# Optimization experiments

Measured on AMD Instinct MI355X. Metric: run time of the kernel, lower is better.

## Reference

```python
import jax, jax.numpy as jnp
import numpy as np

B, T, I, H, O = 1024, 512, 4, 128, 4


def setup_inputs() -> dict:
    key = jax.random.key(0)
    ks = jax.random.split(key, 7)
    s_ih = 1.0 / np.sqrt(H)
    return {
        "x": jax.random.normal(ks[0], (B, T, I), dtype=jnp.float32),
        "W_ih": jax.random.uniform(ks[1], (4 * H, I), jnp.float32, -s_ih, s_ih),
        "W_hh": jax.random.uniform(ks[2], (4 * H, H), jnp.float32, -s_ih, s_ih),
        "b_ih": jax.random.uniform(ks[3], (4 * H,), jnp.float32, -s_ih, s_ih),
        "b_hh": jax.random.uniform(ks[4], (4 * H,), jnp.float32, -s_ih, s_ih),
        "W_fc": jax.random.uniform(ks[5], (O, H), jnp.float32, -s_ih, s_ih),
        "b_fc": jax.random.uniform(ks[6], (O,), jnp.float32, -s_ih, s_ih),
    }


def _lstm_last_hidden(x, W_ih, W_hh, b_ih, b_hh):
    """Single-layer LSTM (PyTorch gate order i,f,g,o); returns h_T of shape (B,H)."""
    Bn = x.shape[0]
    Hn = W_hh.shape[1]
    # Precompute input contributions for all timesteps: (T, B, 4H)
    x_proj = jnp.einsum('bti,gi->tbg', x, W_ih) + (b_ih + b_hh)

    def step(carry, xp_t):
        h, c = carry
        gates = xp_t + h @ W_hh.T  # (B, 4H)
        i_g, f_g, g_g, o_g = jnp.split(gates, 4, axis=-1)
        i_g = jax.nn.sigmoid(i_g)
        f_g = jax.nn.sigmoid(f_g)
        g_g = jnp.tanh(g_g)
        o_g = jax.nn.sigmoid(o_g)
        c = f_g * c + i_g * g_g
        h = o_g * jnp.tanh(c)
        return (h, c), None

    h0 = jnp.zeros((Bn, Hn), x.dtype)
    c0 = jnp.zeros((Bn, Hn), x.dtype)
    (h_T, _), _ = jax.lax.scan(step, (h0, c0), x_proj)
    return h_T


def reference(x, W_ih, W_hh, b_ih, b_hh, W_fc, b_fc):
    # out, _ = lstm(x); last = out[:, -1]; dropout (eval/identity); fc(last)
    last = _lstm_last_hidden(x, W_ih, W_hh, b_ih, b_hh)
    return last @ W_fc.T + b_fc
```

## Files before the change

### kernel.cpp

```cpp
#include <hip/hip_runtime.h>
#include <hip/hip_bf16.h>


#define Tlen 512
#define Iin  4
#define Hdim 128
#define Odim 4

typedef __attribute__((ext_vector_type(8))) short bf16x8;
typedef __attribute__((ext_vector_type(4))) float f32x4;
typedef __attribute__((ext_vector_type(2))) unsigned uint2v;

__device__ __forceinline__ short f2bf(float f) {
  union { float f; unsigned u; } v; v.f = f;
  unsigned u = v.u;
  return (short)((u + 0x7FFFu + ((u >> 16) & 1u)) >> 16);
}
__device__ __forceinline__ unsigned cvt_pk_bf16(float lo, float hi) {
  unsigned r;
  asm("v_cvt_pk_bf16_f32 %0, %1, %2" : "=v"(r) : "v"(lo), "v"(hi));
  return r;
}
__device__ __forceinline__ float ex2(float x) { return __builtin_amdgcn_exp2f(x); }
__device__ __forceinline__ float rcp_(float x) { return __builtin_amdgcn_rcpf(x); }

__global__ __launch_bounds__(512, 2) void lstm_kernel(
    const float* __restrict__ x, const float* __restrict__ W_ih,
    const float* __restrict__ W_hh, const float* __restrict__ b_ih,
    const float* __restrict__ b_hh, const float* __restrict__ W_fc,
    const float* __restrict__ b_fc, float* __restrict__ out) {
  __shared__ alignas(16) short Albuf[2][16][168];
  __shared__ float hfin[16][Hdim];

  const int tid  = threadIdx.x;
  const int wid  = tid >> 6;
  const int lane = tid & 63;
  const int m16  = lane & 15;
  const int grp  = lane >> 4;
  const int bbase = blockIdx.x * 16;
  const float L2E = 1.4426950408889634f;

  bf16x8 Wf[4][5];
  f32x4  c0[4];
#pragma unroll
  for (int q = 0; q < 4; ++q) {
    const float sc = (q == 2) ? 2.0f * L2E : L2E;
    const int gm = q * 128 + wid * 16 + m16;
#pragma unroll
    for (int kc = 0; kc < 4; ++kc) {
      const float* src = W_hh + (size_t)gm * Hdim + kc * 32 + grp * 8;
      bf16x8 w;
#pragma unroll
      for (int e = 0; e < 8; ++e) w[e] = f2bf(src[e] * sc);
      Wf[q][kc] = w;
    }
    bf16x8 w4 = {0, 0, 0, 0, 0, 0, 0, 0};
    if (grp == 0) {
#pragma unroll
      for (int e = 0; e < 4; ++e) w4[e] = f2bf(W_ih[gm * Iin + e] * sc);
    }
    Wf[q][4] = w4;
#pragma unroll
    for (int r = 0; r < 4; ++r) {
      const int gr = q * 128 + wid * 16 + grp * 4 + r;
      c0[q][r] = (b_ih[gr] + b_hh[gr]) * sc;
    }
  }

  for (int i = tid; i < 2 * 16 * 168; i += 512) ((short*)Albuf)[i] = 0;
  __syncthreads();
  if (wid == 0 && lane < 16) {
    const float* xs = x + (size_t)(bbase + m16) * (Tlen * Iin);
    uint2v p;
    p[0] = cvt_pk_bf16(xs[0], xs[1]);
    p[1] = cvt_pk_bf16(xs[2], xs[3]);
    *(uint2v*)&Albuf[0][m16][128] = p;
  }
  __syncthreads();

  float c4[4] = {0.f, 0.f, 0.f, 0.f};
  float hl[4] = {0.f, 0.f, 0.f, 0.f};

  for (int t = 0; t < Tlen; ++t) {
    const int cur = t & 1, nxt = cur ^ 1;

    f32x4 xv = {0.f, 0.f, 0.f, 0.f};
    const bool doX = (wid == 0) && (lane < 16) && (t + 1 < Tlen);
    if (doX)
      xv = *(const f32x4*)(x + (size_t)(bbase + m16) * (Tlen * Iin) + (t + 1) * Iin);

    bf16x8 b[5];
#pragma unroll
    for (int kc = 0; kc < 5; ++kc)
      b[kc] = *(const bf16x8*)&Albuf[cur][m16][kc * 32 + grp * 8];

    f32x4 acc[4];
#pragma unroll
    for (int q = 0; q < 4; ++q)
      acc[q] = __builtin_amdgcn_mfma_f32_16x16x32_bf16(Wf[q][0], b[0], c0[q], 0, 0, 0);
#pragma unroll
    for (int kc = 1; kc < 5; ++kc)
#pragma unroll
      for (int q = 0; q < 4; ++q)
        acc[q] = __builtin_amdgcn_mfma_f32_16x16x32_bf16(Wf[q][kc], b[kc], acc[q], 0, 0, 0);

#pragma unroll
    for (int r = 0; r < 4; ++r) {
      float ig = rcp_(1.0f + ex2(-acc[0][r]));
      float fg = rcp_(1.0f + ex2(-acc[1][r]));
      float gt = __builtin_fmaf(2.0f, rcp_(1.0f + ex2(-acc[2][r])), -1.0f);
      float og = rcp_(1.0f + ex2(-acc[3][r]));
      float c  = __builtin_fmaf(fg, c4[r], ig * gt);
      c4[r] = c;
      float tc = __builtin_fmaf(2.0f, rcp_(1.0f + ex2(-2.8853900817779268f * c)), -1.0f);
      hl[r] = og * tc;
    }
    {
      uint2v p;
      p[0] = cvt_pk_bf16(hl[0], hl[1]);
      p[1] = cvt_pk_bf16(hl[2], hl[3]);
      *(uint2v*)&Albuf[nxt][m16][wid * 16 + grp * 4] = p;
    }
    if (doX) {
      uint2v p;
      p[0] = cvt_pk_bf16(xv[0], xv[1]);
      p[1] = cvt_pk_bf16(xv[2], xv[3]);
      *(uint2v*)&Albuf[nxt][m16][128] = p;
    }
    __syncthreads();
  }

  {
    f32x4 hv;
    hv[0] = hl[0]; hv[1] = hl[1]; hv[2] = hl[2]; hv[3] = hl[3];
    *(f32x4*)&hfin[m16][wid * 16 + grp * 4] = hv;
  }
  __syncthreads();
  if (tid < 64) {
    const int row = tid >> 2, o = tid & 3;
    float s = b_fc[o];
#pragma unroll 8
    for (int k = 0; k < Hdim; ++k) s += hfin[row][k] * W_fc[o * Hdim + k];
    out[(size_t)(bbase + row) * Odim + o] = s;
  }
}

extern "C" void kernel_launch(void* const* d_in, const int* in_sizes, int n_in,
                              void* d_out, int out_size, void* d_ws, size_t ws_size,
                              hipStream_t stream) {
  const float* x    = (const float*)d_in[0];
  const float* W_ih = (const float*)d_in[1];
  const float* W_hh = (const float*)d_in[2];
  const float* b_ih = (const float*)d_in[3];
  const float* b_hh = (const float*)d_in[4];
  const float* W_fc = (const float*)d_in[5];
  const float* b_fc = (const float*)d_in[6];
  float* out = (float*)d_out;
  lstm_kernel<<<64, 512, 0, stream>>>(x, W_ih, W_hh, b_ih, b_hh, W_fc, b_fc, out);
}
```

Before: 426.0 us.

## Precompute next-step input projection off the critical path and interleave gate MFMAs with activations

The x-input contribution is now computed by a separate MFMA with per-lane registers instead of going through shared memory, and it is issued for step t+1 before the barrier. This cuts the recurrent chain to four K-chunks per gate instead of five. Each gate's MFMA chain is followed directly by its sigmoid/tanh so transcendental work can overlap with the next gate's MFMAs. Every wave now loads x every step, which is redundant global traffic, and the minimum-occupancy hint on launch bounds is dropped.

```diff
diff --git a/kernel.cpp b/kernel.cpp
--- a/kernel.cpp
+++ b/kernel.cpp
@@ -10,21 +10,24 @@
 typedef __attribute__((ext_vector_type(8))) short bf16x8;
 typedef __attribute__((ext_vector_type(4))) float f32x4;
 typedef __attribute__((ext_vector_type(2))) unsigned uint2v;
+typedef __attribute__((ext_vector_type(4))) unsigned uint4v;
 
-__device__ __forceinline__ short f2bf(float f) {
+static __device__ __forceinline__ short f2bf(float f) {
   union { float f; unsigned u; } v; v.f = f;
   unsigned u = v.u;
   return (short)((u + 0x7FFFu + ((u >> 16) & 1u)) >> 16);
 }
-__device__ __forceinline__ unsigned cvt_pk_bf16(float lo, float hi) {
+static __device__ __forceinline__ unsigned cvt_pk_bf16(float lo, float hi) {
   unsigned r;
   asm("v_cvt_pk_bf16_f32 %0, %1, %2" : "=v"(r) : "v"(lo), "v"(hi));
   return r;
 }
-__device__ __forceinline__ float ex2(float x) { return __builtin_amdgcn_exp2f(x); }
-__device__ __forceinline__ float rcp_(float x) { return __builtin_amdgcn_rcpf(x); }
+static __device__ __forceinline__ float ex2(float x) { return __builtin_amdgcn_exp2f(x); }
+static __device__ __forceinline__ float rcp_(float x) { return __builtin_amdgcn_rcpf(x); }
 
-__global__ __launch_bounds__(512, 2) void lstm_kernel(
+#define MFMA __builtin_amdgcn_mfma_f32_16x16x32_bf16
+
+__global__ __launch_bounds__(512) void lstm_kernel(
     const float* __restrict__ x, const float* __restrict__ W_ih,
     const float* __restrict__ W_hh, const float* __restrict__ b_ih,
     const float* __restrict__ b_hh, const float* __restrict__ W_fc,
@@ -40,8 +43,9 @@
   const int bbase = blockIdx.x * 16;
   const float L2E = 1.4426950408889634f;
 
-  bf16x8 Wf[4][5];
-  f32x4  c0[4];
+  bf16x8 Wf[4][4];
+  bf16x8 Wx[4];
+  f32x4  c0v[4];
 #pragma unroll
   for (int q = 0; q < 4; ++q) {
     const float sc = (q == 2) ? 2.0f * L2E : L2E;
@@ -59,74 +63,106 @@
 #pragma unroll
       for (int e = 0; e < 4; ++e) w4[e] = f2bf(W_ih[gm * Iin + e] * sc);
     }
-    Wf[q][4] = w4;
+    Wx[q] = w4;
 #pragma unroll
     for (int r = 0; r < 4; ++r) {
       const int gr = q * 128 + wid * 16 + grp * 4 + r;
-      c0[q][r] = (b_ih[gr] + b_hh[gr]) * sc;
+      c0v[q][r] = (b_ih[gr] + b_hh[gr]) * sc;
     }
   }
 
   for (int i = tid; i < 2 * 16 * 168; i += 512) ((short*)Albuf)[i] = 0;
-  __syncthreads();
-  if (wid == 0 && lane < 16) {
-    const float* xs = x + (size_t)(bbase + m16) * (Tlen * Iin);
-    uint2v p;
-    p[0] = cvt_pk_bf16(xs[0], xs[1]);
-    p[1] = cvt_pk_bf16(xs[2], xs[3]);
-    *(uint2v*)&Albuf[0][m16][128] = p;
+
+  const float* xrow = x + (size_t)(bbase + m16) * (Tlen * Iin);
+
+  f32x4 acc0, acc1, acc2, acc3;
+  {
+    f32x4 xv = *(const f32x4*)xrow;
+    uint4v u;
+    u[0] = (grp == 0) ? cvt_pk_bf16(xv[0], xv[1]) : 0u;
+    u[1] = (grp == 0) ? cvt_pk_bf16(xv[2], xv[3]) : 0u;
+    u[2] = 0; u[3] = 0;
+    union { uint4v uu; bf16x8 v; } cst; cst.uu = u;
+    acc0 = MFMA(Wx[0], cst.v, c0v[0], 0, 0, 0);
+    acc1 = MFMA(Wx[1], cst.v, c0v[1], 0, 0, 0);
+    acc2 = MFMA(Wx[2], cst.v, c0v[2], 0, 0, 0);
+    acc3 = MFMA(Wx[3], cst.v, c0v[3], 0, 0, 0);
   }
-  __syncthreads();
 
   float c4[4] = {0.f, 0.f, 0.f, 0.f};
   float hl[4] = {0.f, 0.f, 0.f, 0.f};
+  __syncthreads();
 
   for (int t = 0; t < Tlen; ++t) {
     const int cur = t & 1, nxt = cur ^ 1;
 
-    f32x4 xv = {0.f, 0.f, 0.f, 0.f};
-    const bool doX = (wid == 0) && (lane < 16) && (t + 1 < Tlen);
-    if (doX)
-      xv = *(const f32x4*)(x + (size_t)(bbase + m16) * (Tlen * Iin) + (t + 1) * Iin);
+    bf16x8 b0 = *(const bf16x8*)&Albuf[cur][m16][ 0 + grp * 8];
+    bf16x8 b1 = *(const bf16x8*)&Albuf[cur][m16][32 + grp * 8];
+    bf16x8 b2 = *(const bf16x8*)&Albuf[cur][m16][64 + grp * 8];
+    bf16x8 b3 = *(const bf16x8*)&Albuf[cur][m16][96 + grp * 8];
 
-    bf16x8 b[5];
+    const int tn = (t + 1 < Tlen) ? (t + 1) : (Tlen - 1);
+    f32x4 xv = *(const f32x4*)(xrow + (size_t)tn * Iin);
+
+    acc0 = MFMA(Wf[0][0], b0, acc0, 0, 0, 0);
+    acc0 = MFMA(Wf[0][1], b1, acc0, 0, 0, 0);
+    acc0 = MFMA(Wf[0][2], b2, acc0, 0, 0, 0);
+    acc0 = MFMA(Wf[0][3], b3, acc0, 0, 0, 0);
+    f32x4 si;
 #pragma unroll
-    for (int kc = 0; kc < 5; ++kc)
-      b[kc] = *(const bf16x8*)&Albuf[cur][m16][kc * 32 + grp * 8];
+    for (int r = 0; r < 4; ++r) si[r] = rcp_(1.0f + ex2(-acc0[r]));
 
-    f32x4 acc[4];
+    acc1 = MFMA(Wf[1][0], b0, acc1, 0, 0, 0);
+    acc1 = MFMA(Wf[1][1], b1, acc1, 0, 0, 0);
+    acc1 = MFMA(Wf[1][2], b2, acc1, 0, 0, 0);
+    acc1 = MFMA(Wf[1][3], b3, acc1, 0, 0, 0);
+    f32x4 sf;
 #pragma unroll
-    for (int q = 0; q < 4; ++q)
-      acc[q] = __builtin_amdgcn_mfma_f32_16x16x32_bf16(Wf[q][0], b[0], c0[q], 0, 0, 0);
+    for (int r = 0; r < 4; ++r) sf[r] = rcp_(1.0f + ex2(-acc1[r]));
+
+    acc2 = MFMA(Wf[2][0], b0, acc2, 0, 0, 0);
+    acc2 = MFMA(Wf[2][1], b1, acc2, 0, 0, 0);
+    acc2 = MFMA(Wf[2][2], b2, acc2, 0, 0, 0);
+    acc2 = MFMA(Wf[2][3], b3, acc2, 0, 0, 0);
+    f32x4 gt;
 #pragma unroll
-    for (int kc = 1; kc < 5; ++kc)
+    for (int r = 0; r < 4; ++r)
+      gt[r] = __builtin_fmaf(2.0f, rcp_(1.0f + ex2(-acc2[r])), -1.0f);
+
+    acc3 = MFMA(Wf[3][0], b0, acc3, 0, 0, 0);
+    acc3 = MFMA(Wf[3][1], b1, acc3, 0, 0, 0);
+    acc3 = MFMA(Wf[3][2], b2, acc3, 0, 0, 0);
+    acc3 = MFMA(Wf[3][3], b3, acc3, 0, 0, 0);
+    f32x4 so;
 #pragma unroll
-      for (int q = 0; q < 4; ++q)
-        acc[q] = __builtin_amdgcn_mfma_f32_16x16x32_bf16(Wf[q][kc], b[kc], acc[q], 0, 0, 0);
+    for (int r = 0; r < 4; ++r) so[r] = rcp_(1.0f + ex2(-acc3[r]));
 
 #pragma unroll
     for (int r = 0; r < 4; ++r) {
-      float ig = rcp_(1.0f + ex2(-acc[0][r]));
-      float fg = rcp_(1.0f + ex2(-acc[1][r]));
-      float gt = __builtin_fmaf(2.0f, rcp_(1.0f + ex2(-acc[2][r])), -1.0f);
-      float og = rcp_(1.0f + ex2(-acc[3][r]));
-      float c  = __builtin_fmaf(fg, c4[r], ig * gt);
+      float c = __builtin_fmaf(sf[r], c4[r], si[r] * gt[r]);
       c4[r] = c;
-      float tc = __builtin_fmaf(2.0f, rcp_(1.0f + ex2(-2.8853900817779268f * c)), -1.0f);
-      hl[r] = og * tc;
+      float tc = __builtin_fmaf(
+          2.0f, rcp_(1.0f + ex2(-2.8853900817779268f * c)), -1.0f);
+      hl[r] = so[r] * tc;
     }
+
+    uint2v hp;
+    hp[0] = cvt_pk_bf16(hl[0], hl[1]);
+    hp[1] = cvt_pk_bf16(hl[2], hl[3]);
+
     {
-      uint2v p;
-      p[0] = cvt_pk_bf16(hl[0], hl[1]);
-      p[1] = cvt_pk_bf16(hl[2], hl[3]);
-      *(uint2v*)&Albuf[nxt][m16][wid * 16 + grp * 4] = p;
+      uint4v u;
+      u[0] = (grp == 0) ? cvt_pk_bf16(xv[0], xv[1]) : 0u;
+      u[1] = (grp == 0) ? cvt_pk_bf16(xv[2], xv[3]) : 0u;
+      u[2] = 0; u[3] = 0;
+      union { uint4v uu; bf16x8 v; } cst; cst.uu = u;
+      acc0 = MFMA(Wx[0], cst.v, c0v[0], 0, 0, 0);
+      acc1 = MFMA(Wx[1], cst.v, c0v[1], 0, 0, 0);
+      acc2 = MFMA(Wx[2], cst.v, c0v[2], 0, 0, 0);
+      acc3 = MFMA(Wx[3], cst.v, c0v[3], 0, 0, 0);
     }
-    if (doX) {
-      uint2v p;
-      p[0] = cvt_pk_bf16(xv[0], xv[1]);
-      p[1] = cvt_pk_bf16(xv[2], xv[3]);
-      *(uint2v*)&Albuf[nxt][m16][128] = p;
-    }
+
+    *(uint2v*)&Albuf[nxt][m16][wid * 16 + grp * 4] = hp;
     __syncthreads();
   }
 
```

Result: faster. 400.4 us (-6.0%).
